# Kernel optimization log

Measured on AMD Instinct MI355X. Metric: run time of the kernel, lower is better.

## Reference

```python
import jax, jax.numpy as jnp
import numpy as np

B, L, H = 32, 1024, 512
NEG_INF = -1e30

def setup_inputs() -> dict:
    key = jax.random.key(0)
    k1, k2, k3, k4, k5 = jax.random.split(key, 5)
    c = jax.random.normal(k1, (B, L, H), dtype=jnp.float32)
    c_mask = jax.random.randint(k2, (B, L), 0, 2, dtype=jnp.int32)
    # xavier_uniform-like init scale for [H,1]: sqrt(6/(H+1))
    lim = float(np.sqrt(6.0 / (H + 1)))
    c_weight = jax.random.uniform(k3, (H, 1), minval=-lim, maxval=lim, dtype=jnp.float32)
    q_weight = jax.random.uniform(k4, (H, 1), minval=-lim, maxval=lim, dtype=jnp.float32)
    cq_weight = jax.random.uniform(k5, (1, 1, H), minval=-lim, maxval=lim, dtype=jnp.float32)
    bias = jnp.zeros((1,), dtype=jnp.float32)
    return {"c": c, "c_mask": c_mask, "c_weight": c_weight, "q_weight": q_weight,
            "cq_weight": cq_weight, "bias": bias}

def reference(c, c_mask, c_weight, q_weight, cq_weight, bias):
    m = c_mask.astype(jnp.float32)                     # [B,L]
    # similarity matrix (BiDAF trilinear decomposition), q == c here
    s0 = c @ c_weight                                  # [B,L,1]
    s1 = jnp.swapaxes(c @ q_weight, 1, 2)              # [B,1,L]
    s2 = jnp.einsum('blh,bmh->blm', c * cq_weight, c)  # [B,L,L]
    s = s0 + s1 + s2 + bias                            # [B,L,L]
    mask_row = m[:, None, :]                           # mask over dim=2 (keys)
    mask_col = m[:, :, None]                           # mask over dim=1
    s1p = jax.nn.softmax(mask_row * s + (1.0 - mask_row) * NEG_INF, axis=2)
    s2p = jax.nn.softmax(mask_col * s + (1.0 - mask_col) * NEG_INF, axis=1)
    a = s1p @ c                                        # [B,L,H]
    b = (s1p @ jnp.swapaxes(s2p, 1, 2)) @ c            # [B,L,H]
    return jnp.concatenate([c, a, c * a, c * b], axis=2)  # [B,L,4H]
```

## Files before the change

### kernel.cpp

```cpp
#include <hip/hip_runtime.h>
#include <hip/hip_bf16.h>
#include <stdint.h>

constexpr int Bb = 32;
constexpr int Ll = 1024;
constexpr int Hh = 512;

typedef __attribute__((ext_vector_type(8))) short short8;
typedef __attribute__((ext_vector_type(4))) short short4v;
typedef __attribute__((ext_vector_type(4))) float float4v;
typedef __attribute__((ext_vector_type(4))) int int4v;

__device__ inline short f2bf(float f) {
  union { float f; uint32_t u; } v; v.f = f;
  uint32_t r = (v.u + 0x7FFF + ((v.u >> 16) & 1)) >> 16;
  return (short)r;
}

#define MFMA(a, b, c) __builtin_amdgcn_mfma_f32_16x16x32_bf16(a, b, c, 0, 0, 0)

__device__ inline void gl_lds(const short* g, short* l) {
  __builtin_amdgcn_global_load_lds(
      (const __attribute__((address_space(1))) unsigned int*)g,
      (__attribute__((address_space(3))) unsigned int*)l, 16, 0, 0);
}

template <int ROWS>
__device__ inline void stage(short* lds, const short* g, int sk, int t) {
  const int w = t >> 6;
  const int kbg = (t & 7) ^ ((t >> 3) & 7);
#pragma unroll
  for (int r = 0; r < ROWS / 32; ++r) {
    int row = r * 32 + (t >> 3);
    gl_lds(g + (size_t)row * sk + kbg * 8, lds + (r * 32 + w * 8) * 64);
  }
}

__device__ inline short8 fld(const short* lds, int row, int kb) {
  return *(const short8*)(lds + row * 64 + ((kb ^ (row & 7)) << 3));
}

__global__ __launch_bounds__(256) void k_rowdots(
    const float* __restrict__ c, const float* __restrict__ cw,
    const float* __restrict__ qw, float* __restrict__ s0, float* __restrict__ s1) {
  int row = blockIdx.x * 4 + (threadIdx.x >> 6);
  int lane = threadIdx.x & 63;
  const float* cr = c + (size_t)row * Hh;
  float d0 = 0.f, d1 = 0.f;
#pragma unroll
  for (int i = 0; i < Hh / 64; ++i) {
    int h = lane + i * 64;
    float v = cr[h];
    d0 = fmaf(v, cw[h], d0);
    d1 = fmaf(v, qw[h], d1);
  }
#pragma unroll
  for (int off = 32; off > 0; off >>= 1) {
    d0 += __shfl_down(d0, off);
    d1 += __shfl_down(d1, off);
  }
  if (lane == 0) { s0[row] = d0; s1[row] = d1; }
}

__global__ __launch_bounds__(256) void k_ct(
    const float* __restrict__ c, const float* __restrict__ cq,
    short* __restrict__ cT, short* __restrict__ c16, short* __restrict__ cbq16) {
  const int b = blockIdx.z, h0 = blockIdx.x * 64, l0 = blockIdx.y * 64;
  __shared__ short T[64 * 65];
  const int t = threadIdx.x, rl = t >> 4, c4 = (t & 15) * 4;
  float4v qv = *(const float4v*)&cq[h0 + c4];
#pragma unroll
  for (int p = 0; p < 4; ++p) {
    int ll = rl + p * 16;
    size_t gi = ((size_t)(b * Ll + l0 + ll)) * Hh + h0 + c4;
    float4v v = *(const float4v*)&c[gi];
    short4v o, oq;
#pragma unroll
    for (int j = 0; j < 4; ++j) {
      short bv = f2bf(v[j]);
      T[ll * 65 + c4 + j] = bv;
      o[j] = bv;
      oq[j] = f2bf(v[j] * qv[j]);
    }
    *(short4v*)&c16[gi] = o;
    *(short4v*)&cbq16[gi] = oq;
  }
  __syncthreads();
#pragma unroll
  for (int p = 0; p < 4; ++p) {
    int hh = rl + p * 16;
    short4v o;
#pragma unroll
    for (int j = 0; j < 4; ++j) o[j] = T[(c4 + j) * 65 + hh];
    *(short4v*)&cT[((size_t)(b * Hh + h0 + hh)) * Ll + l0 + c4] = o;
  }
}

__global__ __launch_bounds__(256) void k_sgemm(
    const short* __restrict__ Aq, const short* __restrict__ Bc,
    const float* __restrict__ s0, const float* __restrict__ s1,
    const float* __restrict__ bias, const int* __restrict__ c_mask,
    float* __restrict__ S,
    float* __restrict__ rowpmax, float* __restrict__ rowpsum,
    float* __restrict__ colpmax, float* __restrict__ colpsum) {
  int flat = blockIdx.x + ((blockIdx.y + (blockIdx.z << 3)) << 3);
  flat = ((flat & 7) << 8) | (flat >> 3);
  const int b = flat >> 6, l0 = ((flat >> 3) & 7) << 7, m0 = (flat & 7) << 7;
  __shared__ __align__(16) short As[2][128 * 64];
  __shared__ __align__(16) short Bs[2][128 * 64];
  const int t = threadIdx.x, li = t & 63, w = t >> 6;
  const int wy = w >> 1, wx = w & 1, rr = li & 15, q = li >> 4;
  const short* Ag = Aq + ((size_t)b * Ll + l0) * Hh;
  const short* Bg = Bc + ((size_t)b * Ll + m0) * Hh;
  float4v acc[4][4];
#pragma unroll
  for (int i = 0; i < 4; ++i)
#pragma unroll
    for (int j = 0; j < 4; ++j) acc[i][j] = (float4v){0.f, 0.f, 0.f, 0.f};
  stage<128>(As[0], Ag, Hh, t);
  stage<128>(Bs[0], Bg, Hh, t);
  __syncthreads();
  for (int it = 0; it < Hh / 64; ++it) {
    if (it + 1 < Hh / 64) {
      stage<128>(As[(it + 1) & 1], Ag + (it + 1) * 64, Hh, t);
      stage<128>(Bs[(it + 1) & 1], Bg + (it + 1) * 64, Hh, t);
    }
    const short* Ab = As[it & 1];
    const short* Bbuf = Bs[it & 1];
#pragma unroll
    for (int ks = 0; ks < 2; ++ks) {
      int kb = ks * 4 + q;
      short8 af[4], bf4[4];
#pragma unroll
      for (int mt = 0; mt < 4; ++mt) af[mt] = fld(Ab, wy * 64 + mt * 16 + rr, kb);
#pragma unroll
      for (int nt = 0; nt < 4; ++nt) bf4[nt] = fld(Bbuf, wx * 64 + nt * 16 + rr, kb);
#pragma unroll
      for (int mt = 0; mt < 4; ++mt)
#pragma unroll
        for (int nt = 0; nt < 4; ++nt)
          acc[mt][nt] = MFMA(af[mt], bf4[nt], acc[mt][nt]);
    }
    __syncthreads();
  }
  const float bsc = bias[0];
  float s1v[4]; int mkm[4];
#pragma unroll
  for (int nt = 0; nt < 4; ++nt) {
    int m = m0 + wx * 64 + nt * 16 + rr;
    s1v[nt] = s1[b * Ll + m] + bsc;
    mkm[nt] = c_mask[b * Ll + m];
  }
  int mkl[4][4];
#pragma unroll
  for (int mt = 0; mt < 4; ++mt)
#pragma unroll
    for (int i = 0; i < 4; ++i) {
      int l = l0 + wy * 64 + mt * 16 + q * 4 + i;
      float s0v = s0[b * Ll + l];
      mkl[mt][i] = c_mask[b * Ll + l];
#pragma unroll
      for (int nt = 0; nt < 4; ++nt) acc[mt][nt][i] += s0v + s1v[nt];
    }
  float* Sb = S + (size_t)b * Ll * Ll;
#pragma unroll
  for (int nt = 0; nt < 4; ++nt) {
    int m = m0 + wx * 64 + nt * 16 + rr;
#pragma unroll
    for (int mt = 0; mt < 4; ++mt)
#pragma unroll
      for (int i = 0; i < 4; ++i) {
        int l = l0 + wy * 64 + mt * 16 + q * 4 + i;
        Sb[(size_t)l * Ll + m] = acc[mt][nt][i];
      }
  }
  float* red = (float*)As;
  const size_t rbase = (size_t)(m0 >> 7) * (Bb * Ll) + (size_t)b * Ll + l0;
  const size_t cbase = (size_t)(l0 >> 7) * (Bb * Ll) + (size_t)b * Ll + m0;
  float rv[16];
#pragma unroll
  for (int mt = 0; mt < 4; ++mt)
#pragma unroll
    for (int i = 0; i < 4; ++i) {
      float v = -INFINITY;
#pragma unroll
      for (int nt = 0; nt < 4; ++nt) v = mkm[nt] ? fmaxf(v, acc[mt][nt][i]) : v;
      rv[mt * 4 + i] = v;
    }
#pragma unroll
  for (int off = 1; off < 16; off <<= 1)
#pragma unroll
    for (int j = 0; j < 16; ++j) rv[j] = fmaxf(rv[j], __shfl_xor(rv[j], off));
  if (rr == 0)
#pragma unroll
    for (int j = 0; j < 16; ++j)
      red[wx * 128 + wy * 64 + (j >> 2) * 16 + q * 4 + (j & 3)] = rv[j];
  __syncthreads();
  if (t < 128) {
    float M = fmaxf(red[t], red[128 + t]);
    red[t] = M;
    rowpmax[rbase + t] = M;
  }
  __syncthreads();
#pragma unroll
  for (int mt = 0; mt < 4; ++mt)
#pragma unroll
    for (int i = 0; i < 4; ++i) {
      float M = red[wy * 64 + mt * 16 + q * 4 + i];
      float sacc = 0.f;
      if (M > -INFINITY) {
#pragma unroll
        for (int nt = 0; nt < 4; ++nt)
          sacc += mkm[nt] ? __expf(acc[mt][nt][i] - M) : 0.f;
      }
      rv[mt * 4 + i] = sacc;
    }
#pragma unroll
  for (int off = 1; off < 16; off <<= 1)
#pragma unroll
    for (int j = 0; j < 16; ++j) rv[j] += __shfl_xor(rv[j], off);
  __syncthreads();
  if (rr == 0)
#pragma unroll
    for (int j = 0; j < 16; ++j)
      red[wx * 128 + wy * 64 + (j >> 2) * 16 + q * 4 + (j & 3)] = rv[j];
  __syncthreads();
  if (t < 128) rowpsum[rbase + t] = red[t] + red[128 + t];
  float cv[4];
#pragma unroll
  for (int nt = 0; nt < 4; ++nt) {
    float v = -INFINITY;
#pragma unroll
    for (int mt = 0; mt < 4; ++mt)
#pragma unroll
      for (int i = 0; i < 4; ++i) v = mkl[mt][i] ? fmaxf(v, acc[mt][nt][i]) : v;
    cv[nt] = v;
  }
#pragma unroll
  for (int nt = 0; nt < 4; ++nt) {
    cv[nt] = fmaxf(cv[nt], __shfl_xor(cv[nt], 16));
    cv[nt] = fmaxf(cv[nt], __shfl_xor(cv[nt], 32));
  }
  __syncthreads();
  if (q == 0)
#pragma unroll
    for (int nt = 0; nt < 4; ++nt) red[wy * 128 + wx * 64 + nt * 16 + rr] = cv[nt];
  __syncthreads();
  if (t < 128) {
    float M = fmaxf(red[t], red[128 + t]);
    red[t] = M;
    colpmax[cbase + t] = M;
  }
  __syncthreads();
#pragma unroll
  for (int nt = 0; nt < 4; ++nt) {
    float M = red[wx * 64 + nt * 16 + rr];
    float sacc = 0.f;
    if (M > -INFINITY) {
#pragma unroll
      for (int mt = 0; mt < 4; ++mt)
#pragma unroll
        for (int i = 0; i < 4; ++i)
          sacc += mkl[mt][i] ? __expf(acc[mt][nt][i] - M) : 0.f;
    }
    cv[nt] = sacc;
  }
#pragma unroll
  for (int nt = 0; nt < 4; ++nt) {
    cv[nt] += __shfl_xor(cv[nt], 16);
    cv[nt] += __shfl_xor(cv[nt], 32);
  }
  __syncthreads();
  if (q == 0)
#pragma unroll
    for (int nt = 0; nt < 4; ++nt) red[wy * 128 + wx * 64 + nt * 16 + rr] = cv[nt];
  __syncthreads();
  if (t < 128) colpsum[cbase + t] = red[t] + red[128 + t];
}

__global__ __launch_bounds__(256) void k_comb2(
    const float* __restrict__ rpm, const float* __restrict__ rps,
    const float* __restrict__ cpm, const float* __restrict__ cps,
    float* __restrict__ rmax, float* __restrict__ rrcp,
    float* __restrict__ cmax, float* __restrict__ crcp) {
  int i = blockIdx.x * 256 + threadIdx.x;
  const float* pmax = blockIdx.y ? cpm : rpm;
  const float* psum = blockIdx.y ? cps : rps;
  float* omax = blockIdx.y ? cmax : rmax;
  float* orcp = blockIdx.y ? crcp : rrcp;
  float M = -INFINITY;
#pragma unroll
  for (int k = 0; k < 8; ++k) M = fmaxf(M, pmax[k * (Bb * Ll) + i]);
  float s = 0.f;
#pragma unroll
  for (int k = 0; k < 8; ++k) {
    float pm = pmax[k * (Bb * Ll) + i];
    if (pm > -INFINITY) s += psum[k * (Bb * Ll) + i] * __expf(pm - M);
  }
  omax[i] = M;
  orcp[i] = 1.f / s;
}

__global__ __launch_bounds__(256) void k_p12(
    const float* __restrict__ S, const int* __restrict__ c_mask,
    const float* __restrict__ rowmax, const float* __restrict__ rowrcp,
    const float* __restrict__ colmax, const float* __restrict__ colrcp,
    short* __restrict__ P1, short* __restrict__ P2T) {
  const int b = blockIdx.z, m0 = blockIdx.x * 64, l0 = blockIdx.y * 64;
  __shared__ short T[64 * 65];
  const int t = threadIdx.x, rl = t >> 4, c4 = (t & 15) * 4;
  const float* Sb = S + (size_t)b * Ll * Ll;
  float4v cm = *(const float4v*)&colmax[b * Ll + m0 + c4];
  float4v cr = *(const float4v*)&colrcp[b * Ll + m0 + c4];
  int4v mkm = *(const int4v*)&c_mask[b * Ll + m0 + c4];
#pragma unroll
  for (int p = 0; p < 4; ++p) {
    int ll = rl + p * 16;
    int gl = b * Ll + l0 + ll;
    int mkl = c_mask[gl];
    float rm = rowmax[gl], rrc = rowrcp[gl];
    float4v v = *(const float4v*)&Sb[(size_t)(l0 + ll) * Ll + m0 + c4];
    short4v o1;
#pragma unroll
    for (int j = 0; j < 4; ++j) {
      o1[j] = mkm[j] ? f2bf(__expf(v[j] - rm) * rrc) : (short)0;
      T[ll * 65 + c4 + j] = mkl ? f2bf(__expf(v[j] - cm[j]) * cr[j]) : (short)0;
    }
    *(short4v*)&P1[(size_t)gl * Ll + m0 + c4] = o1;
  }
  __syncthreads();
#pragma unroll
  for (int p = 0; p < 4; ++p) {
    int mm = rl + p * 16;
    short4v o;
#pragma unroll
    for (int j = 0; j < 4; ++j) o[j] = T[(c4 + j) * 65 + mm];
    *(short4v*)&P2T[((size_t)(b * Ll + m0 + mm)) * Ll + l0 + c4] = o;
  }
}

__global__ __launch_bounds__(256) void k_ugemm(
    const short* __restrict__ P2T, const short* __restrict__ cT,
    short* __restrict__ uT) {
  int flat = blockIdx.x + ((blockIdx.y + (blockIdx.z << 3)) << 2);
  flat = ((flat & 7) << 7) | (flat >> 3);
  const int b = flat >> 5, m0 = ((flat >> 2) & 7) << 7, h0 = (flat & 3) << 7;
  __shared__ __align__(16) short As[2][128 * 64];
  __shared__ __align__(16) short Bs[2][128 * 64];
  const int t = threadIdx.x, li = t & 63, w = t >> 6;
  const int wy = w >> 1, wx = w & 1, rr = li & 15, q = li >> 4;
  const short* Ag = P2T + ((size_t)b * Ll + m0) * Ll;
  const short* Bg = cT + ((size_t)b * Hh + h0) * Ll;
  float4v acc[4][4];
#pragma unroll
  for (int i = 0; i < 4; ++i)
#pragma unroll
    for (int j = 0; j < 4; ++j) acc[i][j] = (float4v){0.f, 0.f, 0.f, 0.f};
  stage<128>(As[0], Ag, Ll, t);
  stage<128>(Bs[0], Bg, Ll, t);
  __syncthreads();
  for (int it = 0; it < Ll / 64; ++it) {
    if (it + 1 < Ll / 64) {
      stage<128>(As[(it + 1) & 1], Ag + (it + 1) * 64, Ll, t);
      stage<128>(Bs[(it + 1) & 1], Bg + (it + 1) * 64, Ll, t);
    }
    const short* Ab = As[it & 1];
    const short* Bbuf = Bs[it & 1];
#pragma unroll
    for (int ks = 0; ks < 2; ++ks) {
      int kb = ks * 4 + q;
      short8 af[4], bf4[4];
#pragma unroll
      for (int mt = 0; mt < 4; ++mt) af[mt] = fld(Ab, wy * 64 + mt * 16 + rr, kb);
#pragma unroll
      for (int nt = 0; nt < 4; ++nt) bf4[nt] = fld(Bbuf, wx * 64 + nt * 16 + rr, kb);
#pragma unroll
      for (int mt = 0; mt < 4; ++mt)
#pragma unroll
        for (int nt = 0; nt < 4; ++nt)
          acc[mt][nt] = MFMA(af[mt], bf4[nt], acc[mt][nt]);
    }
    __syncthreads();
  }
#pragma unroll
  for (int nt = 0; nt < 4; ++nt) {
    int h = h0 + wx * 64 + nt * 16 + rr;
#pragma unroll
    for (int mt = 0; mt < 4; ++mt) {
      int mb = m0 + wy * 64 + mt * 16 + q * 4;
      short4v o;
#pragma unroll
      for (int i = 0; i < 4; ++i) o[i] = f2bf(acc[mt][nt][i]);
      *(short4v*)&uT[((size_t)b * Hh + h) * Ll + mb] = o;
    }
  }
}

__global__ __launch_bounds__(256) void k_abgemm(
    const short* __restrict__ P1, const short* __restrict__ cT,
    const short* __restrict__ uT, const float* __restrict__ c,
    float* __restrict__ out) {
  int flat = blockIdx.x + ((blockIdx.y + (blockIdx.z << 3)) << 3);
  flat = ((flat & 7) << 8) | (flat >> 3);
  const int b = flat >> 6, l0 = ((flat >> 3) & 7) << 7, h0 = (flat & 7) << 6;
  __shared__ __align__(16) short As[2][128 * 64];
  __shared__ __align__(16) short B1s[2][64 * 64];
  __shared__ __align__(16) short B2s[2][64 * 64];
  const int t = threadIdx.x, li = t & 63, w = t >> 6;
  const int wy = w >> 1, wx = w & 1, rr = li & 15, q = li >> 4;
  const short* Ag = P1 + ((size_t)b * Ll + l0) * Ll;
  const short* B1g = cT + ((size_t)b * Hh + h0) * Ll;
  const short* B2g = uT + ((size_t)b * Hh + h0) * Ll;
  float4v aa[4][2], ab[4][2];
#pragma unroll
  for (int i = 0; i < 4; ++i)
#pragma unroll
    for (int j = 0; j < 2; ++j) {
      aa[i][j] = (float4v){0.f, 0.f, 0.f, 0.f};
      ab[i][j] = (float4v){0.f, 0.f, 0.f, 0.f};
    }
  stage<128>(As[0], Ag, Ll, t);
  stage<64>(B1s[0], B1g, Ll, t);
  stage<64>(B2s[0], B2g, Ll, t);
  __syncthreads();
  for (int it = 0; it < Ll / 64; ++it) {
    if (it + 1 < Ll / 64) {
      stage<128>(As[(it + 1) & 1], Ag + (it + 1) * 64, Ll, t);
      stage<64>(B1s[(it + 1) & 1], B1g + (it + 1) * 64, Ll, t);
      stage<64>(B2s[(it + 1) & 1], B2g + (it + 1) * 64, Ll, t);
    }
    const short* Ab = As[it & 1];
    const short* B1b = B1s[it & 1];
    const short* B2b = B2s[it & 1];
#pragma unroll
    for (int ks = 0; ks < 2; ++ks) {
      int kb = ks * 4 + q;
      short8 af[4], b1[2], b2[2];
#pragma unroll
      for (int mt = 0; mt < 4; ++mt) af[mt] = fld(Ab, wy * 64 + mt * 16 + rr, kb);
#pragma unroll
      for (int nt = 0; nt < 2; ++nt) {
        b1[nt] = fld(B1b, wx * 32 + nt * 16 + rr, kb);
        b2[nt] = fld(B2b, wx * 32 + nt * 16 + rr, kb);
      }
#pragma unroll
      for (int mt = 0; mt < 4; ++mt)
#pragma unroll
        for (int nt = 0; nt < 2; ++nt) {
          aa[mt][nt] = MFMA(af[mt], b1[nt], aa[mt][nt]);
          ab[mt][nt] = MFMA(af[mt], b2[nt], ab[mt][nt]);
        }
    }
    __syncthreads();
  }
#pragma unroll
  for (int nt = 0; nt < 2; ++nt) {
    int h = h0 + wx * 32 + nt * 16 + rr;
#pragma unroll
    for (int mt = 0; mt < 4; ++mt) {
#pragma unroll
      for (int i = 0; i < 4; ++i) {
        int l = l0 + wy * 64 + mt * 16 + q * 4 + i;
        float cv = c[((size_t)b * Ll + l) * Hh + h];
        size_t ob = ((size_t)b * Ll + l) * (size_t)(4 * Hh);
        float av = aa[mt][nt][i], bv = ab[mt][nt][i];
        out[ob + h] = cv;
        out[ob + Hh + h] = av;
        out[ob + 2 * Hh + h] = cv * av;
        out[ob + 3 * Hh + h] = cv * bv;
      }
    }
  }
}

extern "C" void kernel_launch(void* const* d_in, const int* in_sizes, int n_in,
                              void* d_out, int out_size, void* d_ws, size_t ws_size,
                              hipStream_t stream) {
  const float* c = (const float*)d_in[0];
  const int* c_mask = (const int*)d_in[1];
  const float* c_weight = (const float*)d_in[2];
  const float* q_weight = (const float*)d_in[3];
  const float* cq = (const float*)d_in[4];
  const float* bias = (const float*)d_in[5];
  float* out = (float*)d_out;

  char* ws = (char*)d_ws;
  float* S = (float*)ws;
  short* uT = (short*)ws;
  short* cT16 = (short*)(ws + 134217728ull);
  short* c16 = (short*)(ws + 167772160ull);
  short* P1 = (short*)(ws + 167772160ull);
  short* cbq16 = (short*)(ws + 201326592ull);
  short* P2T = (short*)(ws + 234881024ull);
  float* rowpmax = (float*)(ws + 234881024ull);
  float* rowpsum = (float*)(ws + 234881024ull + 1048576ull);
  float* colpmax = (float*)(ws + 234881024ull + 2097152ull);
  float* colpsum = (float*)(ws + 234881024ull + 3145728ull);
  float* st = (float*)(ws + 301989888ull);
  float* s0 = st;
  float* s1 = st + 32768;
  float* rowmax = st + 65536;
  float* rowrcp = st + 98304;
  float* colmax = st + 131072;
  float* colrcp = st + 163840;

  k_rowdots<<<dim3(Bb * Ll / 4), dim3(256), 0, stream>>>(c, c_weight, q_weight, s0, s1);
  k_ct<<<dim3(Hh / 64, Ll / 64, Bb), dim3(256), 0, stream>>>(c, cq, cT16, c16, cbq16);
  k_sgemm<<<dim3(Ll / 128, Ll / 128, Bb), dim3(256), 0, stream>>>(
      cbq16, c16, s0, s1, bias, c_mask, S, rowpmax, rowpsum, colpmax, colpsum);
  k_comb2<<<dim3(Bb * Ll / 256, 2), dim3(256), 0, stream>>>(
      rowpmax, rowpsum, colpmax, colpsum, rowmax, rowrcp, colmax, colrcp);
  k_p12<<<dim3(Ll / 64, Ll / 64, Bb), dim3(256), 0, stream>>>(
      S, c_mask, rowmax, rowrcp, colmax, colrcp, P1, P2T);
  k_ugemm<<<dim3(Hh / 128, Ll / 128, Bb), dim3(256), 0, stream>>>(P2T, cT16, uT);
  k_abgemm<<<dim3(Hh / 64, Ll / 128, Bb), dim3(256), 0, stream>>>(P1, cT16, uT, c, out);
}
```

Measured before the change: 719.4 us.

## Replace LDS-staged GEMM tiles with direct global-to-register MFMA operand loads

The three GEMM kernels no longer stage tiles into shared memory with double buffering and barriers. Each lane now loads its MFMA operand fragments straight from global memory using per-row pointers, relying on L1/L2 for reuse between waves. This removes the LDS traffic and __syncthreads, and allows higher occupancy through new launch_bounds minimum-block hints. The cost is lost explicit prefetch overlap and more redundant global loads, since rows are shared by two waves. The per-lane 16-byte loads along strided rows are also less coalesced.

```diff
diff --git a/kernel.cpp b/kernel.cpp
--- a/kernel.cpp
+++ b/kernel.cpp
@@ -18,27 +18,6 @@
 }
 
 #define MFMA(a, b, c) __builtin_amdgcn_mfma_f32_16x16x32_bf16(a, b, c, 0, 0, 0)
-
-__device__ inline void gl_lds(const short* g, short* l) {
-  __builtin_amdgcn_global_load_lds(
-      (const __attribute__((address_space(1))) unsigned int*)g,
-      (__attribute__((address_space(3))) unsigned int*)l, 16, 0, 0);
-}
-
-template <int ROWS>
-__device__ inline void stage(short* lds, const short* g, int sk, int t) {
-  const int w = t >> 6;
-  const int kbg = (t & 7) ^ ((t >> 3) & 7);
-#pragma unroll
-  for (int r = 0; r < ROWS / 32; ++r) {
-    int row = r * 32 + (t >> 3);
-    gl_lds(g + (size_t)row * sk + kbg * 8, lds + (r * 32 + w * 8) * 64);
-  }
-}
-
-__device__ inline short8 fld(const short* lds, int row, int kb) {
-  return *(const short8*)(lds + row * 64 + ((kb ^ (row & 7)) << 3));
-}
 
 __global__ __launch_bounds__(256) void k_rowdots(
     const float* __restrict__ c, const float* __restrict__ cw,
@@ -96,7 +75,7 @@
   }
 }
 
-__global__ __launch_bounds__(256) void k_sgemm(
+__global__ __launch_bounds__(256, 3) void k_sgemm(
     const short* __restrict__ Aq, const short* __restrict__ Bc,
     const float* __restrict__ s0, const float* __restrict__ s1,
     const float* __restrict__ bias, const int* __restrict__ c_mask,
@@ -106,42 +85,34 @@
   int flat = blockIdx.x + ((blockIdx.y + (blockIdx.z << 3)) << 3);
   flat = ((flat & 7) << 8) | (flat >> 3);
   const int b = flat >> 6, l0 = ((flat >> 3) & 7) << 7, m0 = (flat & 7) << 7;
-  __shared__ __align__(16) short As[2][128 * 64];
-  __shared__ __align__(16) short Bs[2][128 * 64];
+  __shared__ float red[256];
   const int t = threadIdx.x, li = t & 63, w = t >> 6;
   const int wy = w >> 1, wx = w & 1, rr = li & 15, q = li >> 4;
-  const short* Ag = Aq + ((size_t)b * Ll + l0) * Hh;
-  const short* Bg = Bc + ((size_t)b * Ll + m0) * Hh;
+  const int ko = q * 8;
+  const short* Ap[4];
+  const short* Bp[4];
+#pragma unroll
+  for (int mt = 0; mt < 4; ++mt)
+    Ap[mt] = Aq + ((size_t)(b * Ll + l0 + wy * 64 + mt * 16 + rr)) * Hh + ko;
+#pragma unroll
+  for (int nt = 0; nt < 4; ++nt)
+    Bp[nt] = Bc + ((size_t)(b * Ll + m0 + wx * 64 + nt * 16 + rr)) * Hh + ko;
   float4v acc[4][4];
 #pragma unroll
   for (int i = 0; i < 4; ++i)
 #pragma unroll
     for (int j = 0; j < 4; ++j) acc[i][j] = (float4v){0.f, 0.f, 0.f, 0.f};
-  stage<128>(As[0], Ag, Hh, t);
-  stage<128>(Bs[0], Bg, Hh, t);
-  __syncthreads();
-  for (int it = 0; it < Hh / 64; ++it) {
-    if (it + 1 < Hh / 64) {
-      stage<128>(As[(it + 1) & 1], Ag + (it + 1) * 64, Hh, t);
-      stage<128>(Bs[(it + 1) & 1], Bg + (it + 1) * 64, Hh, t);
-    }
-    const short* Ab = As[it & 1];
-    const short* Bbuf = Bs[it & 1];
-#pragma unroll
-    for (int ks = 0; ks < 2; ++ks) {
-      int kb = ks * 4 + q;
-      short8 af[4], bf4[4];
-#pragma unroll
-      for (int mt = 0; mt < 4; ++mt) af[mt] = fld(Ab, wy * 64 + mt * 16 + rr, kb);
-#pragma unroll
-      for (int nt = 0; nt < 4; ++nt) bf4[nt] = fld(Bbuf, wx * 64 + nt * 16 + rr, kb);
-#pragma unroll
-      for (int mt = 0; mt < 4; ++mt)
-#pragma unroll
-        for (int nt = 0; nt < 4; ++nt)
-          acc[mt][nt] = MFMA(af[mt], bf4[nt], acc[mt][nt]);
-    }
-    __syncthreads();
+  for (int kk = 0; kk < Hh; kk += 32) {
+    short8 af[4], bf4[4];
+#pragma unroll
+    for (int mt = 0; mt < 4; ++mt) af[mt] = *(const short8*)(Ap[mt] + kk);
+#pragma unroll
+    for (int nt = 0; nt < 4; ++nt) bf4[nt] = *(const short8*)(Bp[nt] + kk);
+#pragma unroll
+    for (int mt = 0; mt < 4; ++mt)
+#pragma unroll
+      for (int nt = 0; nt < 4; ++nt)
+        acc[mt][nt] = MFMA(af[mt], bf4[nt], acc[mt][nt]);
   }
   const float bsc = bias[0];
   float s1v[4]; int mkm[4];
@@ -174,7 +145,6 @@
         Sb[(size_t)l * Ll + m] = acc[mt][nt][i];
       }
   }
-  float* red = (float*)As;
   const size_t rbase = (size_t)(m0 >> 7) * (Bb * Ll) + (size_t)b * Ll + l0;
   const size_t cbase = (size_t)(l0 >> 7) * (Bb * Ll) + (size_t)b * Ll + m0;
   float rv[16];
@@ -339,48 +309,39 @@
   }
 }
 
-__global__ __launch_bounds__(256) void k_ugemm(
+__global__ __launch_bounds__(256, 4) void k_ugemm(
     const short* __restrict__ P2T, const short* __restrict__ cT,
     short* __restrict__ uT) {
   int flat = blockIdx.x + ((blockIdx.y + (blockIdx.z << 3)) << 2);
   flat = ((flat & 7) << 7) | (flat >> 3);
   const int b = flat >> 5, m0 = ((flat >> 2) & 7) << 7, h0 = (flat & 3) << 7;
-  __shared__ __align__(16) short As[2][128 * 64];
-  __shared__ __align__(16) short Bs[2][128 * 64];
   const int t = threadIdx.x, li = t & 63, w = t >> 6;
   const int wy = w >> 1, wx = w & 1, rr = li & 15, q = li >> 4;
-  const short* Ag = P2T + ((size_t)b * Ll + m0) * Ll;
-  const short* Bg = cT + ((size_t)b * Hh + h0) * Ll;
+  const int ko = q * 8;
+  const short* Ap[4];
+  const short* Bp[4];
+#pragma unroll
+  for (int mt = 0; mt < 4; ++mt)
+    Ap[mt] = P2T + ((size_t)(b * Ll + m0 + wy * 64 + mt * 16 + rr)) * Ll + ko;
+#pragma unroll
+  for (int nt = 0; nt < 4; ++nt)
+    Bp[nt] = cT + ((size_t)(b * Hh + h0 + wx * 64 + nt * 16 + rr)) * Ll + ko;
   float4v acc[4][4];
 #pragma unroll
   for (int i = 0; i < 4; ++i)
 #pragma unroll
     for (int j = 0; j < 4; ++j) acc[i][j] = (float4v){0.f, 0.f, 0.f, 0.f};
-  stage<128>(As[0], Ag, Ll, t);
-  stage<128>(Bs[0], Bg, Ll, t);
-  __syncthreads();
-  for (int it = 0; it < Ll / 64; ++it) {
-    if (it + 1 < Ll / 64) {
-      stage<128>(As[(it + 1) & 1], Ag + (it + 1) * 64, Ll, t);
-      stage<128>(Bs[(it + 1) & 1], Bg + (it + 1) * 64, Ll, t);
-    }
-    const short* Ab = As[it & 1];
-    const short* Bbuf = Bs[it & 1];
-#pragma unroll
-    for (int ks = 0; ks < 2; ++ks) {
-      int kb = ks * 4 + q;
-      short8 af[4], bf4[4];
-#pragma unroll
-      for (int mt = 0; mt < 4; ++mt) af[mt] = fld(Ab, wy * 64 + mt * 16 + rr, kb);
-#pragma unroll
-      for (int nt = 0; nt < 4; ++nt) bf4[nt] = fld(Bbuf, wx * 64 + nt * 16 + rr, kb);
-#pragma unroll
-      for (int mt = 0; mt < 4; ++mt)
-#pragma unroll
-        for (int nt = 0; nt < 4; ++nt)
-          acc[mt][nt] = MFMA(af[mt], bf4[nt], acc[mt][nt]);
-    }
-    __syncthreads();
+  for (int kk = 0; kk < Ll; kk += 32) {
+    short8 af[4], bf4[4];
+#pragma unroll
+    for (int mt = 0; mt < 4; ++mt) af[mt] = *(const short8*)(Ap[mt] + kk);
+#pragma unroll
+    for (int nt = 0; nt < 4; ++nt) bf4[nt] = *(const short8*)(Bp[nt] + kk);
+#pragma unroll
+    for (int mt = 0; mt < 4; ++mt)
+#pragma unroll
+      for (int nt = 0; nt < 4; ++nt)
+        acc[mt][nt] = MFMA(af[mt], bf4[nt], acc[mt][nt]);
   }
 #pragma unroll
   for (int nt = 0; nt < 4; ++nt) {
@@ -396,21 +357,27 @@
   }
 }
 
-__global__ __launch_bounds__(256) void k_abgemm(
+__global__ __launch_bounds__(256, 4) void k_abgemm(
     const short* __restrict__ P1, const short* __restrict__ cT,
     const short* __restrict__ uT, const float* __restrict__ c,
     float* __restrict__ out) {
   int flat = blockIdx.x + ((blockIdx.y + (blockIdx.z << 3)) << 3);
   flat = ((flat & 7) << 8) | (flat >> 3);
   const int b = flat >> 6, l0 = ((flat >> 3) & 7) << 7, h0 = (flat & 7) << 6;
-  __shared__ __align__(16) short As[2][128 * 64];
-  __shared__ __align__(16) short B1s[2][64 * 64];
-  __shared__ __align__(16) short B2s[2][64 * 64];
   const int t = threadIdx.x, li = t & 63, w = t >> 6;
   const int wy = w >> 1, wx = w & 1, rr = li & 15, q = li >> 4;
-  const short* Ag = P1 + ((size_t)b * Ll + l0) * Ll;
-  const short* B1g = cT + ((size_t)b * Hh + h0) * Ll;
-  const short* B2g = uT + ((size_t)b * Hh + h0) * Ll;
+  const int ko = q * 8;
+  const short* Ap[4];
+  const short* B1p[2];
+  const short* B2p[2];
+#pragma unroll
+  for (int mt = 0; mt < 4; ++mt)
+    Ap[mt] = P1 + ((size_t)(b * Ll + l0 + wy * 64 + mt * 16 + rr)) * Ll + ko;
+#pragma unroll
+  for (int nt = 0; nt < 2; ++nt) {
+    B1p[nt] = cT + ((size_t)(b * Hh + h0 + wx * 32 + nt * 16 + rr)) * Ll + ko;
+    B2p[nt] = uT + ((size_t)(b * Hh + h0 + wx * 32 + nt * 16 + rr)) * Ll + ko;
+  }
   float4v aa[4][2], ab[4][2];
 #pragma unroll
   for (int i = 0; i < 4; ++i)
@@ -419,39 +386,22 @@
       aa[i][j] = (float4v){0.f, 0.f, 0.f, 0.f};
       ab[i][j] = (float4v){0.f, 0.f, 0.f, 0.f};
     }
-  stage<128>(As[0], Ag, Ll, t);
-  stage<64>(B1s[0], B1g, Ll, t);
-  stage<64>(B2s[0], B2g, Ll, t);
-  __syncthreads();
-  for (int it = 0; it < Ll / 64; ++it) {
-    if (it + 1 < Ll / 64) {
-      stage<128>(As[(it + 1) & 1], Ag + (it + 1) * 64, Ll, t);
-      stage<64>(B1s[(it + 1) & 1], B1g + (it + 1) * 64, Ll, t);
-      stage<64>(B2s[(it + 1) & 1], B2g + (it + 1) * 64, Ll, t);
-    }
-    const short* Ab = As[it & 1];
-    const short* B1b = B1s[it & 1];
-    const short* B2b = B2s[it & 1];
-#pragma unroll
-    for (int ks = 0; ks < 2; ++ks) {
-      int kb = ks * 4 + q;
-      short8 af[4], b1[2], b2[2];
-#pragma unroll
-      for (int mt = 0; mt < 4; ++mt) af[mt] = fld(Ab, wy * 64 + mt * 16 + rr, kb);
+  for (int kk = 0; kk < Ll; kk += 32) {
+    short8 af[4], b1[2], b2[2];
+#pragma unroll
+    for (int mt = 0; mt < 4; ++mt) af[mt] = *(const short8*)(Ap[mt] + kk);
+#pragma unroll
+    for (int nt = 0; nt < 2; ++nt) {
+      b1[nt] = *(const short8*)(B1p[nt] + kk);
+      b2[nt] = *(const short8*)(B2p[nt] + kk);
+    }
+#pragma unroll
+    for (int mt = 0; mt < 4; ++mt)
 #pragma unroll
       for (int nt = 0; nt < 2; ++nt) {
-        b1[nt] = fld(B1b, wx * 32 + nt * 16 + rr, kb);
-        b2[nt] = fld(B2b, wx * 32 + nt * 16 + rr, kb);
+        aa[mt][nt] = MFMA(af[mt], b1[nt], aa[mt][nt]);
+        ab[mt][nt] = MFMA(af[mt], b2[nt], ab[mt][nt]);
       }
-#pragma unroll
-      for (int mt = 0; mt < 4; ++mt)
-#pragma unroll
-        for (int nt = 0; nt < 2; ++nt) {
-          aa[mt][nt] = MFMA(af[mt], b1[nt], aa[mt][nt]);
-          ab[mt][nt] = MFMA(af[mt], b2[nt], ab[mt][nt]);
-        }
-    }
-    __syncthreads();
   }
 #pragma unroll
   for (int nt = 0; nt < 2; ++nt) {
```

New measurement: 1.028 ms. 42.9% more time.
